# Kernel tuning notes

Measured on AMD Instinct MI355X. Metric: run time of the kernel, lower is better.

Reference implementation:

```python
import jax, jax.numpy as jnp
import numpy as np

B, S, D = 2, 2048, 1024
H, HKV, HD = 16, 4, 64
REP = H // HKV
THETA = 10000.0
NEG = -1e9


def _rope_tables(seq_len, head_dim, theta):
    inv = 1.0 / (theta ** (np.arange(0, head_dim, 2, dtype=np.float32) / head_dim))
    t = np.arange(seq_len, dtype=np.float32)
    f = np.outer(t, inv)  # [S, HD/2]
    return jnp.asarray(np.cos(f)), jnp.asarray(np.sin(f))


def setup_inputs() -> dict:
    key = jax.random.key(0)
    kx, kq, kk, kv, ko = jax.random.split(key, 5)
    s = 0.02
    x = jax.random.normal(kx, (B, S, D), dtype=jnp.float32)
    wq = jax.random.normal(kq, (H * HD, D), dtype=jnp.float32) * s
    wk = jax.random.normal(kk, (HKV * HD, D), dtype=jnp.float32) * s
    wv = jax.random.normal(kv, (HKV * HD, D), dtype=jnp.float32) * s
    wo = jax.random.normal(ko, (D, H * HD), dtype=jnp.float32) * s
    freqs_cos, freqs_sin = _rope_tables(S, HD, THETA)
    mask = jnp.triu(jnp.full((S, S), NEG, dtype=jnp.float32), k=1)  # causal additive
    return {"x": x, "wq": wq, "wk": wk, "wv": wv, "wo": wo,
            "freqs_cos": freqs_cos, "freqs_sin": freqs_sin, "mask": mask}


def _apply_rope(t, cos, sin):
    # t: [B, S, nH, HD]; treat last dim as HD/2 complex pairs, multiply by e^{i f}
    tf = t.astype(jnp.float32).reshape(*t.shape[:-1], HD // 2, 2)
    tr, ti = tf[..., 0], tf[..., 1]
    c = cos[None, :, None, :]
    s = sin[None, :, None, :]
    outr = tr * c - ti * s
    outi = tr * s + ti * c
    out = jnp.stack([outr, outi], axis=-1).reshape(*t.shape)
    return out.astype(t.dtype)


def reference(x, wq, wk, wv, wo, freqs_cos, freqs_sin, mask):
    xq = jnp.einsum('bsd,od->bso', x, wq).reshape(B, S, H, HD)
    xk = jnp.einsum('bsd,od->bso', x, wk).reshape(B, S, HKV, HD)
    xv = jnp.einsum('bsd,od->bso', x, wv).reshape(B, S, HKV, HD)
    xq = _apply_rope(xq, freqs_cos, freqs_sin)
    xk = _apply_rope(xk, freqs_cos, freqs_sin)
    # GQA: group query heads [B,S,HKV,REP,HD]; broadcast KV instead of physical repeat
    xqg = xq.reshape(B, S, HKV, REP, HD)
    scores = jnp.einsum('bqgrd,bkgd->bgrqk', xqg, xk) / jnp.sqrt(jnp.float32(HD))
    scores = scores + mask[None, None, None, :, :]
    attn = jax.nn.softmax(scores.astype(jnp.float32), axis=-1).astype(xq.dtype)
    out = jnp.einsum('bgrqk,bkgd->bqgrd', attn, xv)  # [B,S,HKV,REP,HD]
    out = out.reshape(B, S, H * HD)
    return jnp.einsum('bso,do->bsd', out, wo)
```

## Files before the change

kernel.cpp:

```cpp
#include <hip/hip_runtime.h>


#define B_   2
#define S_   2048
#define D_   1024
#define H_   16
#define HKV_ 4
#define HD_  64

typedef __attribute__((ext_vector_type(8))) short bf16x8;
typedef __attribute__((ext_vector_type(4))) float f32x4;
typedef __attribute__((ext_vector_type(4))) short short4v;

__device__ __forceinline__ short f2bf(float f) {
    unsigned u = __builtin_bit_cast(unsigned, f);
    u += 0x7fffu + ((u >> 16) & 1u);
    return (short)(u >> 16);
}

__device__ __forceinline__ void gll16(const void* g, void* l) {
    __builtin_amdgcn_global_load_lds(
        (const __attribute__((address_space(1))) unsigned int*)g,
        (__attribute__((address_space(3))) unsigned int*)l, 16, 0, 0);
}

__global__ void cast_f32_bf16(const float* __restrict__ in, short* __restrict__ out, int n) {
    int i = (blockIdx.x * blockDim.x + threadIdx.x) * 4;
    if (i >= n) return;
    float4 v = *(const float4*)(in + i);
    short4v o = { f2bf(v.x), f2bf(v.y), f2bf(v.z), f2bf(v.w) };
    *(short4v*)(out + i) = o;
}

__global__ void rope_cast(const float* __restrict__ xqkv, short* __restrict__ out,
                          const float* __restrict__ fc, const float* __restrict__ fs,
                          int nh, int colofs) {
    int idx = blockIdx.x * blockDim.x + threadIdx.x;
    int p    = idx & 31;
    int rest = idx >> 5;
    int h    = rest & (nh - 1);
    int s    = (rest / nh) & (S_ - 1);
    int b    = rest / (nh * S_);
    size_t row = (size_t)b * S_ + s;
    const float* src = xqkv + row * 1536 + colofs + h * 64 + 2 * p;
    float tr = src[0], ti = src[1];
    float c = fc[s * 32 + p], sn = fs[s * 32 + p];
    short* dst = out + (row * nh + h) * 64 + 2 * p;
    dst[0] = f2bf(tr * c - ti * sn);
    dst[1] = f2bf(tr * sn + ti * c);
}

__global__ __launch_bounds__(256) void transpose_cast_v(const float* __restrict__ xqkv,
                                                        short* __restrict__ vt) {
    __shared__ float tl[64][65];
    const int t = threadIdx.x;
    const int s0 = blockIdx.x * 64, g = blockIdx.y, b = blockIdx.z;
#pragma unroll
    for (int i = 0; i < 16; ++i) {
        int e = t + i * 256, r = e >> 6, d = e & 63;
        tl[r][d] = xqkv[(size_t)(b * S_ + s0 + r) * 1536 + 1280 + g * 64 + d];
    }
    __syncthreads();
#pragma unroll
    for (int i = 0; i < 16; ++i) {
        int e = t + i * 256, dr = e >> 6, sc = e & 63;
        vt[(size_t)((b * HKV_ + g) * 64 + dr) * S_ + s0 + sc] = f2bf(tl[sc][dr]);
    }
}

__global__ __launch_bounds__(256, 2) void gemm_bf16_nt(
    const short* __restrict__ A, const short* __restrict__ Bw,
    float* __restrict__ C, int N, int K) {
    __shared__ short A_l[128 * 64];
    __shared__ short B_l[128 * 64];
    const int t = threadIdx.x, ln = t & 63, wid = t >> 6;
    const int wr = wid >> 1, wc = wid & 1;
    const int r0 = blockIdx.y * 128, c0 = blockIdx.x * 128;
    f32x4 acc[4][4] = {};
    for (int k0 = 0; k0 < K; k0 += 64) {
#pragma unroll
        for (int i = 0; i < 4; ++i) {
            int row = wid * 32 + i * 8 + (ln >> 3);
            int sc_ = ((ln & 7) ^ (row & 7)) * 8;
            gll16(A + (size_t)(r0 + row) * K + k0 + sc_, A_l + wid * 2048 + i * 512);
            gll16(Bw + (size_t)(c0 + row) * K + k0 + sc_, B_l + wid * 2048 + i * 512);
        }
        __syncthreads();
#pragma unroll
        for (int kk = 0; kk < 2; ++kk) {
            bf16x8 af[4], bfr[4];
#pragma unroll
            for (int mi = 0; mi < 4; ++mi) {
                int row = wr * 64 + mi * 16 + (ln & 15);
                int addr = row * 128 + (((kk * 4 + (ln >> 4)) ^ (row & 7)) << 4);
                af[mi] = *(const bf16x8*)((const char*)A_l + addr);
            }
#pragma unroll
            for (int ni = 0; ni < 4; ++ni) {
                int col = wc * 64 + ni * 16 + (ln & 15);
                int addr = col * 128 + (((kk * 4 + (ln >> 4)) ^ (col & 7)) << 4);
                bfr[ni] = *(const bf16x8*)((const char*)B_l + addr);
            }
#pragma unroll
            for (int mi = 0; mi < 4; ++mi)
#pragma unroll
                for (int ni = 0; ni < 4; ++ni)
                    acc[mi][ni] = __builtin_amdgcn_mfma_f32_16x16x32_bf16(
                        af[mi], bfr[ni], acc[mi][ni], 0, 0, 0);
        }
        __syncthreads();
    }
#pragma unroll
    for (int mi = 0; mi < 4; ++mi)
#pragma unroll
        for (int ni = 0; ni < 4; ++ni)
#pragma unroll
            for (int rg = 0; rg < 4; ++rg) {
                int r = r0 + wr * 64 + mi * 16 + (ln >> 4) * 4 + rg;
                int c = c0 + wc * 64 + ni * 16 + (ln & 15);
                C[(size_t)r * N + c] = acc[mi][ni][rg];
            }
}

__global__ __launch_bounds__(256, 2) void attn_mfma(
    const short* __restrict__ Qb, const short* __restrict__ Kb,
    const short* __restrict__ Vt, short* __restrict__ Ob) {
    __shared__ short K_l[64 * 64];
    __shared__ short V_l[64 * 64];
    __shared__ short P_l[4 * 16 * 64];
    const int t = threadIdx.x, ln = t & 63, wid = t >> 6;
    const int qt = (int)gridDim.x - 1 - (int)blockIdx.x;
    const int h = blockIdx.y, b = blockIdx.z, g = h >> 2;
    const int q0 = qt * 64;
    const int lg = ln >> 4, q = ln & 15;
    const int qrow = q0 + wid * 16 + q;

    bf16x8 qf[2];
#pragma unroll
    for (int kk = 0; kk < 2; ++kk)
        qf[kk] = *(const bf16x8*)(Qb + ((size_t)(b * S_ + qrow) * H_ + h) * HD_ + kk * 32 + lg * 8);

    f32x4 acc[4] = {};
    float mrun = -3.0e38f, lsum = 0.f;

    for (int kt = 0; kt <= qt; ++kt) {
        const int k0 = kt * 64;
#pragma unroll
        for (int i = 0; i < 2; ++i) {
            int row = wid * 16 + i * 8 + (ln >> 3);
            int sc_ = ((ln & 7) ^ (row & 7)) * 8;
            gll16(Kb + ((size_t)(b * S_ + k0 + row) * HKV_ + g) * HD_ + sc_,
                  K_l + wid * 1024 + i * 512);
            gll16(Vt + ((size_t)((b * HKV_ + g) * 64 + row)) * S_ + k0 + sc_,
                  V_l + wid * 1024 + i * 512);
        }
        __syncthreads();

        f32x4 st[4] = {};
#pragma unroll
        for (int kk = 0; kk < 2; ++kk)
#pragma unroll
            for (int r = 0; r < 4; ++r) {
                int row = r * 16 + q;
                int addr = row * 128 + (((kk * 4 + lg) ^ (row & 7)) << 4);
                bf16x8 ka = *(const bf16x8*)((const char*)K_l + addr);
                st[r] = __builtin_amdgcn_mfma_f32_16x16x32_bf16(ka, qf[kk], st[r], 0, 0, 0);
            }

        const bool diag = (kt == qt);
        const int qg = q0 + wid * 16 + q;
        float mloc = -3.0e38f;
#pragma unroll
        for (int r = 0; r < 4; ++r)
#pragma unroll
            for (int j = 0; j < 4; ++j) {
                float v = st[r][j] * 0.125f;
                if (diag && (k0 + r * 16 + lg * 4 + j > qg)) v = -3.0e38f;
                st[r][j] = v;
                mloc = fmaxf(mloc, v);
            }
        mloc = fmaxf(mloc, __shfl_xor(mloc, 16));
        mloc = fmaxf(mloc, __shfl_xor(mloc, 32));
        float nm = fmaxf(mrun, mloc);
        float scl = __expf(mrun - nm);
        float rsum = 0.f;
#pragma unroll
        for (int r = 0; r < 4; ++r)
#pragma unroll
            for (int j = 0; j < 4; ++j) {
                float e = __expf(st[r][j] - nm);
                st[r][j] = e;
                rsum += e;
            }
        rsum += __shfl_xor(rsum, 16);
        rsum += __shfl_xor(rsum, 32);
        lsum = lsum * scl + rsum;
        mrun = nm;
#pragma unroll
        for (int d = 0; d < 4; ++d)
#pragma unroll
            for (int j = 0; j < 4; ++j) acc[d][j] *= scl;

#pragma unroll
        for (int r = 0; r < 4; ++r) {
            short4v pk = { f2bf(st[r][0]), f2bf(st[r][1]), f2bf(st[r][2]), f2bf(st[r][3]) };
            int sb = wid * 2048 + q * 128 + ((r * 32 + lg * 8) ^ ((q & 7) << 4));
            *(short4v*)((char*)P_l + sb) = pk;
        }

#pragma unroll
        for (int kk2 = 0; kk2 < 2; ++kk2) {
            int pba = wid * 2048 + q * 128 + (((kk2 * 4 + lg) ^ (q & 7)) << 4);
            bf16x8 pb = *(const bf16x8*)((const char*)P_l + pba);
#pragma unroll
            for (int d = 0; d < 4; ++d) {
                int row = d * 16 + q;
                int addr = row * 128 + (((kk2 * 4 + lg) ^ (row & 7)) << 4);
                bf16x8 va = *(const bf16x8*)((const char*)V_l + addr);
                acc[d] = __builtin_amdgcn_mfma_f32_16x16x32_bf16(va, pb, acc[d], 0, 0, 0);
            }
        }
        __syncthreads();
    }

    float inv = 1.f / lsum;
#pragma unroll
    for (int d = 0; d < 4; ++d) {
        short4v o4 = { f2bf(acc[d][0] * inv), f2bf(acc[d][1] * inv),
                       f2bf(acc[d][2] * inv), f2bf(acc[d][3] * inv) };
        *(short4v*)(Ob + ((size_t)(b * S_ + qrow) * H_ + h) * HD_ + d * 16 + lg * 4) = o4;
    }
}

extern "C" void kernel_launch(void* const* d_in, const int* in_sizes, int n_in,
                              void* d_out, int out_size, void* d_ws, size_t ws_size,
                              hipStream_t stream)
{
    const float* x  = (const float*)d_in[0];
    const float* wq = (const float*)d_in[1];
    const float* wk = (const float*)d_in[2];
    const float* wv = (const float*)d_in[3];
    const float* wo = (const float*)d_in[4];
    const float* fc = (const float*)d_in[5];
    const float* fs = (const float*)d_in[6];
    float* out = (float*)d_out;

    char* ws = (char*)d_ws;
    short* wqkvb = (short*)(ws);
    short* wob   = (short*)(ws + 3145728);
    short* xb    = (short*)(ws + 5242880);
    float* xqkv  = (float*)(ws + 13631488);
    short* qb    = (short*)(ws + 38797312);
    short* kb    = (short*)(ws + 47185920);
    short* vtb   = (short*)(ws + 49283072);
    short* aob   = xb;

    cast_f32_bf16<<<4096, 256, 0, stream>>>(x,  xb,               4194304);
    cast_f32_bf16<<<1024, 256, 0, stream>>>(wq, wqkvb,            1048576);
    cast_f32_bf16<<<256,  256, 0, stream>>>(wk, wqkvb + 1048576,  262144);
    cast_f32_bf16<<<256,  256, 0, stream>>>(wv, wqkvb + 1310720,  262144);
    cast_f32_bf16<<<1024, 256, 0, stream>>>(wo, wob,              1048576);

    gemm_bf16_nt<<<dim3(12, 32), 256, 0, stream>>>(xb, wqkvb, xqkv, 1536, 1024);

    rope_cast<<<8192, 256, 0, stream>>>(xqkv, qb, fc, fs, 16, 0);
    rope_cast<<<2048, 256, 0, stream>>>(xqkv, kb, fc, fs, 4, 1024);
    transpose_cast_v<<<dim3(32, 4, 2), 256, 0, stream>>>(xqkv, vtb);

    attn_mfma<<<dim3(32, 16, 2), 256, 0, stream>>>(qb, kb, vtb, aob);

    gemm_bf16_nt<<<dim3(8, 32), 256, 0, stream>>>(aob, wob, out, 1024, 1024);
}
```

Baseline: 224.7 us.

## Fuse casts, fuse RoPE into QKV GEMM epilogue, double-buffer attention KV loads

New measurement: 212.3 us. 5.5% less time.

```diff
diff --git a/kernel.cpp b/kernel.cpp
--- a/kernel.cpp
+++ b/kernel.cpp
@@ -24,47 +24,122 @@
         (__attribute__((address_space(3))) unsigned int*)l, 16, 0, 0);
 }
 
-__global__ void cast_f32_bf16(const float* __restrict__ in, short* __restrict__ out, int n) {
-    int i = (blockIdx.x * blockDim.x + threadIdx.x) * 4;
-    if (i >= n) return;
-    float4 v = *(const float4*)(in + i);
+__global__ void cast_all(const float* __restrict__ x,  const float* __restrict__ wq,
+                         const float* __restrict__ wk, const float* __restrict__ wv,
+                         const float* __restrict__ wo,
+                         short* __restrict__ xb, short* __restrict__ wqkvb,
+                         short* __restrict__ wob) {
+    int i4 = blockIdx.x * blockDim.x + threadIdx.x;
+    const float* src;
+    short* dst;
+    int base;
+    if (i4 < 1048576)      { src = x;  dst = xb;    base = 0; }
+    else if (i4 < 1310720) { src = wq; dst = wqkvb; base = 1048576; }
+    else if (i4 < 1376256) { src = wk; dst = wqkvb + 1048576; base = 1310720; }
+    else if (i4 < 1441792) { src = wv; dst = wqkvb + 1310720; base = 1376256; }
+    else                   { src = wo; dst = wob;   base = 1441792; }
+    int e = (i4 - base) * 4;
+    float4 v = *(const float4*)(src + e);
     short4v o = { f2bf(v.x), f2bf(v.y), f2bf(v.z), f2bf(v.w) };
-    *(short4v*)(out + i) = o;
-}
-
-__global__ void rope_cast(const float* __restrict__ xqkv, short* __restrict__ out,
-                          const float* __restrict__ fc, const float* __restrict__ fs,
-                          int nh, int colofs) {
-    int idx = blockIdx.x * blockDim.x + threadIdx.x;
-    int p    = idx & 31;
-    int rest = idx >> 5;
-    int h    = rest & (nh - 1);
-    int s    = (rest / nh) & (S_ - 1);
-    int b    = rest / (nh * S_);
-    size_t row = (size_t)b * S_ + s;
-    const float* src = xqkv + row * 1536 + colofs + h * 64 + 2 * p;
-    float tr = src[0], ti = src[1];
-    float c = fc[s * 32 + p], sn = fs[s * 32 + p];
-    short* dst = out + (row * nh + h) * 64 + 2 * p;
-    dst[0] = f2bf(tr * c - ti * sn);
-    dst[1] = f2bf(tr * sn + ti * c);
-}
-
-__global__ __launch_bounds__(256) void transpose_cast_v(const float* __restrict__ xqkv,
-                                                        short* __restrict__ vt) {
-    __shared__ float tl[64][65];
+    *(short4v*)(dst + e) = o;
+}
+
+__global__ __launch_bounds__(256, 2) void gemm_qkv(
+    const short* __restrict__ A, const short* __restrict__ W,
+    const float* __restrict__ fc, const float* __restrict__ fs,
+    short* __restrict__ qb, short* __restrict__ kb, short* __restrict__ vb) {
+    __shared__ short A_l[128 * 64];
+    __shared__ short B_l[128 * 64];
+    const int t = threadIdx.x, ln = t & 63, wid = t >> 6;
+    const int wr = wid >> 1, wc = wid & 1;
+    const int r0 = blockIdx.y * 128, c0 = blockIdx.x * 128;
+    const int K = 1024;
+    f32x4 acc[4][4] = {};
+    for (int k0 = 0; k0 < K; k0 += 64) {
+#pragma unroll
+        for (int i = 0; i < 4; ++i) {
+            int row = wid * 32 + i * 8 + (ln >> 3);
+            int sc_ = ((ln & 7) ^ (row & 7)) * 8;
+            gll16(A + (size_t)(r0 + row) * K + k0 + sc_, A_l + wid * 2048 + i * 512);
+            gll16(W + (size_t)(c0 + row) * K + k0 + sc_, B_l + wid * 2048 + i * 512);
+        }
+        __syncthreads();
+#pragma unroll
+        for (int kk = 0; kk < 2; ++kk) {
+            bf16x8 af[4], bfr[4];
+#pragma unroll
+            for (int mi = 0; mi < 4; ++mi) {
+                int row = wr * 64 + mi * 16 + (ln & 15);
+                int addr = row * 128 + (((kk * 4 + (ln >> 4)) ^ (row & 7)) << 4);
+                af[mi] = *(const bf16x8*)((const char*)A_l + addr);
+            }
+#pragma unroll
+            for (int ni = 0; ni < 4; ++ni) {
+                int col = wc * 64 + ni * 16 + (ln & 15);
+                int addr = col * 128 + (((kk * 4 + (ln >> 4)) ^ (col & 7)) << 4);
+                bfr[ni] = *(const bf16x8*)((const char*)B_l + addr);
+            }
+#pragma unroll
+            for (int mi = 0; mi < 4; ++mi)
+#pragma unroll
+                for (int ni = 0; ni < 4; ++ni)
+                    acc[mi][ni] = __builtin_amdgcn_mfma_f32_16x16x32_bf16(
+                        af[mi], bfr[ni], acc[mi][ni], 0, 0, 0);
+        }
+        __syncthreads();
+    }
+
+    const float QSCALE = 0.18033688f;
+    const int region = (c0 < 1024) ? 0 : (c0 < 1280 ? 1 : 2);
+#pragma unroll
+    for (int mi = 0; mi < 4; ++mi)
+#pragma unroll
+        for (int ni = 0; ni < 4; ++ni) {
+            int col = c0 + wc * 64 + ni * 16 + (ln & 15);
+#pragma unroll
+            for (int rg = 0; rg < 4; ++rg) {
+                int row = r0 + wr * 64 + mi * 16 + (ln >> 4) * 4 + rg;
+                int s = row & (S_ - 1), b = row >> 11;
+                float v = acc[mi][ni][rg];
+                if (region == 2) {
+                    int cc = col - 1280, g = cc >> 6, d = cc & 63;
+                    vb[((size_t)(b * S_ + s) * HKV_ + g) * HD_ + d] = f2bf(v);
+                } else {
+                    int cc = region ? (col - 1024) : col;
+                    int d = cc & 63, p = d >> 1;
+                    float c = fc[s * 32 + p], sn = fs[s * 32 + p];
+                    float pv = __shfl_xor(v, 1);
+                    float sgn = (col & 1) ? sn : -sn;
+                    float o = v * c + sgn * pv;
+                    if (region == 0) {
+                        o *= QSCALE;
+                        qb[((size_t)(b * S_ + s) * H_ + (cc >> 6)) * HD_ + d] = f2bf(o);
+                    } else {
+                        kb[((size_t)(b * S_ + s) * HKV_ + (cc >> 6)) * HD_ + d] = f2bf(o);
+                    }
+                }
+            }
+        }
+}
+
+__global__ __launch_bounds__(256) void transpose_v(const short* __restrict__ vb,
+                                                   short* __restrict__ vt) {
+    __shared__ short tl[64][68];
     const int t = threadIdx.x;
     const int s0 = blockIdx.x * 64, g = blockIdx.y, b = blockIdx.z;
 #pragma unroll
-    for (int i = 0; i < 16; ++i) {
-        int e = t + i * 256, r = e >> 6, d = e & 63;
-        tl[r][d] = xqkv[(size_t)(b * S_ + s0 + r) * 1536 + 1280 + g * 64 + d];
+    for (int i = 0; i < 4; ++i) {
+        int e = t + i * 256, r = e >> 4, c4 = (e & 15) * 4;
+        *(short4v*)&tl[r][c4] =
+            *(const short4v*)(vb + ((size_t)(b * S_ + s0 + r) * HKV_ + g) * HD_ + c4);
     }
     __syncthreads();
-#pragma unroll
-    for (int i = 0; i < 16; ++i) {
-        int e = t + i * 256, dr = e >> 6, sc = e & 63;
-        vt[(size_t)((b * HKV_ + g) * 64 + dr) * S_ + s0 + sc] = f2bf(tl[sc][dr]);
+    const int dr = t >> 2, sc0 = (t & 3) * 16;
+#pragma unroll
+    for (int i = 0; i < 4; ++i) {
+        short4v o = { tl[sc0 + i * 4 + 0][dr], tl[sc0 + i * 4 + 1][dr],
+                      tl[sc0 + i * 4 + 2][dr], tl[sc0 + i * 4 + 3][dr] };
+        *(short4v*)(vt + ((size_t)((b * HKV_ + g) * 64 + dr)) * S_ + s0 + sc0 + i * 4) = o;
     }
 }
 
@@ -122,18 +197,20 @@
             }
 }
 
-__global__ __launch_bounds__(256, 2) void attn_mfma(
+__global__ __launch_bounds__(256, 4) void attn_mfma(
     const short* __restrict__ Qb, const short* __restrict__ Kb,
     const short* __restrict__ Vt, short* __restrict__ Ob) {
-    __shared__ short K_l[64 * 64];
-    __shared__ short V_l[64 * 64];
-    __shared__ short P_l[4 * 16 * 64];
+    __shared__ short K_l[2][64 * 64];
+    __shared__ short V_l[2][64 * 64];
+    __shared__ short P_l[4][16 * 64];
     const int t = threadIdx.x, ln = t & 63, wid = t >> 6;
     const int qt = (int)gridDim.x - 1 - (int)blockIdx.x;
     const int h = blockIdx.y, b = blockIdx.z, g = h >> 2;
     const int q0 = qt * 64;
     const int lg = ln >> 4, q = ln & 15;
     const int qrow = q0 + wid * 16 + q;
+    const int stg_row = wid * 16 + (ln >> 3);
+    const int stg_sc0 = (ln & 7) * 8;
 
     bf16x8 qf[2];
 #pragma unroll
@@ -143,19 +220,28 @@
     f32x4 acc[4] = {};
     float mrun = -3.0e38f, lsum = 0.f;
 
+#define STAGE(KT, BUF)                                                              \
+    {                                                                               \
+        const int k0s = (KT) * 64;                                                  \
+        _Pragma("unroll")                                                           \
+        for (int i = 0; i < 2; ++i) {                                               \
+            int row = stg_row + i * 8;                                              \
+            int sc_ = stg_sc0 ^ ((row & 7) * 8);                                    \
+            gll16(Kb + ((size_t)(b * S_ + k0s + row) * HKV_ + g) * HD_ + sc_,       \
+                  &K_l[BUF][wid * 1024 + i * 512]);                                 \
+            gll16(Vt + ((size_t)((b * HKV_ + g) * 64 + row)) * S_ + k0s + sc_,      \
+                  &V_l[BUF][wid * 1024 + i * 512]);                                 \
+        }                                                                           \
+    }
+
+    STAGE(0, 0);
+    __syncthreads();
+    int cur = 0;
+
     for (int kt = 0; kt <= qt; ++kt) {
+        if (kt < qt) STAGE(kt + 1, cur ^ 1);
+
         const int k0 = kt * 64;
-#pragma unroll
-        for (int i = 0; i < 2; ++i) {
-            int row = wid * 16 + i * 8 + (ln >> 3);
-            int sc_ = ((ln & 7) ^ (row & 7)) * 8;
-            gll16(Kb + ((size_t)(b * S_ + k0 + row) * HKV_ + g) * HD_ + sc_,
-                  K_l + wid * 1024 + i * 512);
-            gll16(Vt + ((size_t)((b * HKV_ + g) * 64 + row)) * S_ + k0 + sc_,
-                  V_l + wid * 1024 + i * 512);
-        }
-        __syncthreads();
-
         f32x4 st[4] = {};
 #pragma unroll
         for (int kk = 0; kk < 2; ++kk)
@@ -163,65 +249,76 @@
             for (int r = 0; r < 4; ++r) {
                 int row = r * 16 + q;
                 int addr = row * 128 + (((kk * 4 + lg) ^ (row & 7)) << 4);
-                bf16x8 ka = *(const bf16x8*)((const char*)K_l + addr);
+                bf16x8 ka = *(const bf16x8*)((const char*)&K_l[cur][0] + addr);
                 st[r] = __builtin_amdgcn_mfma_f32_16x16x32_bf16(ka, qf[kk], st[r], 0, 0, 0);
             }
 
         const bool diag = (kt == qt);
-        const int qg = q0 + wid * 16 + q;
         float mloc = -3.0e38f;
-#pragma unroll
-        for (int r = 0; r < 4; ++r)
-#pragma unroll
-            for (int j = 0; j < 4; ++j) {
-                float v = st[r][j] * 0.125f;
-                if (diag && (k0 + r * 16 + lg * 4 + j > qg)) v = -3.0e38f;
-                st[r][j] = v;
-                mloc = fmaxf(mloc, v);
-            }
+        if (diag) {
+#pragma unroll
+            for (int r = 0; r < 4; ++r)
+#pragma unroll
+                for (int j = 0; j < 4; ++j) {
+                    if (k0 + r * 16 + lg * 4 + j > qrow) st[r][j] = -3.0e38f;
+                    mloc = fmaxf(mloc, st[r][j]);
+                }
+        } else {
+#pragma unroll
+            for (int r = 0; r < 4; ++r)
+#pragma unroll
+                for (int j = 0; j < 4; ++j) mloc = fmaxf(mloc, st[r][j]);
+        }
         mloc = fmaxf(mloc, __shfl_xor(mloc, 16));
         mloc = fmaxf(mloc, __shfl_xor(mloc, 32));
-        float nm = fmaxf(mrun, mloc);
-        float scl = __expf(mrun - nm);
+
+        if (!__all(mloc <= mrun + 8.f)) {
+            float nm = fmaxf(mrun, mloc);
+            float scl = __builtin_amdgcn_exp2f(mrun - nm);
+            lsum *= scl;
+#pragma unroll
+            for (int d = 0; d < 4; ++d)
+#pragma unroll
+                for (int j = 0; j < 4; ++j) acc[d][j] *= scl;
+            mrun = nm;
+        }
+
         float rsum = 0.f;
 #pragma unroll
         for (int r = 0; r < 4; ++r)
 #pragma unroll
             for (int j = 0; j < 4; ++j) {
-                float e = __expf(st[r][j] - nm);
+                float e = __builtin_amdgcn_exp2f(st[r][j] - mrun);
                 st[r][j] = e;
                 rsum += e;
             }
         rsum += __shfl_xor(rsum, 16);
         rsum += __shfl_xor(rsum, 32);
-        lsum = lsum * scl + rsum;
-        mrun = nm;
-#pragma unroll
-        for (int d = 0; d < 4; ++d)
-#pragma unroll
-            for (int j = 0; j < 4; ++j) acc[d][j] *= scl;
+        lsum += rsum;
 
 #pragma unroll
         for (int r = 0; r < 4; ++r) {
             short4v pk = { f2bf(st[r][0]), f2bf(st[r][1]), f2bf(st[r][2]), f2bf(st[r][3]) };
-            int sb = wid * 2048 + q * 128 + ((r * 32 + lg * 8) ^ ((q & 7) << 4));
-            *(short4v*)((char*)P_l + sb) = pk;
+            int sb = q * 128 + ((r * 32 + lg * 8) ^ ((q & 7) << 4));
+            *(short4v*)((char*)&P_l[wid][0] + sb) = pk;
         }
 
 #pragma unroll
         for (int kk2 = 0; kk2 < 2; ++kk2) {
-            int pba = wid * 2048 + q * 128 + (((kk2 * 4 + lg) ^ (q & 7)) << 4);
-            bf16x8 pb = *(const bf16x8*)((const char*)P_l + pba);
+            int pba = q * 128 + (((kk2 * 4 + lg) ^ (q & 7)) << 4);
+            bf16x8 pb = *(const bf16x8*)((const char*)&P_l[wid][0] + pba);
 #pragma unroll
             for (int d = 0; d < 4; ++d) {
                 int row = d * 16 + q;
                 int addr = row * 128 + (((kk2 * 4 + lg) ^ (row & 7)) << 4);
-                bf16x8 va = *(const bf16x8*)((const char*)V_l + addr);
+                bf16x8 va = *(const bf16x8*)((const char*)&V_l[cur][0] + addr);
                 acc[d] = __builtin_amdgcn_mfma_f32_16x16x32_bf16(va, pb, acc[d], 0, 0, 0);
             }
         }
         __syncthreads();
-    }
+        cur ^= 1;
+    }
+#undef STAGE
 
     float inv = 1.f / lsum;
 #pragma unroll
@@ -249,23 +346,17 @@
     short* wqkvb = (short*)(ws);
     short* wob   = (short*)(ws + 3145728);
     short* xb    = (short*)(ws + 5242880);
-    float* xqkv  = (float*)(ws + 13631488);
-    short* qb    = (short*)(ws + 38797312);
-    short* kb    = (short*)(ws + 47185920);
-    short* vtb   = (short*)(ws + 49283072);
+    short* qb    = (short*)(ws + 13631488);
+    short* kb    = (short*)(ws + 22020096);
+    short* vb    = (short*)(ws + 24117248);
+    short* vtb   = (short*)(ws + 26214400);
     short* aob   = xb;
 
-    cast_f32_bf16<<<4096, 256, 0, stream>>>(x,  xb,               4194304);
-    cast_f32_bf16<<<1024, 256, 0, stream>>>(wq, wqkvb,            1048576);
-    cast_f32_bf16<<<256,  256, 0, stream>>>(wk, wqkvb + 1048576,  262144);
-    cast_f32_bf16<<<256,  256, 0, stream>>>(wv, wqkvb + 1310720,  262144);
-    cast_f32_bf16<<<1024, 256, 0, stream>>>(wo, wob,              1048576);
-
-    gemm_bf16_nt<<<dim3(12, 32), 256, 0, stream>>>(xb, wqkvb, xqkv, 1536, 1024);
-
-    rope_cast<<<8192, 256, 0, stream>>>(xqkv, qb, fc, fs, 16, 0);
-    rope_cast<<<2048, 256, 0, stream>>>(xqkv, kb, fc, fs, 4, 1024);
-    transpose_cast_v<<<dim3(32, 4, 2), 256, 0, stream>>>(xqkv, vtb);
+    cast_all<<<6656, 256, 0, stream>>>(x, wq, wk, wv, wo, xb, wqkvb, wob);
+
+    gemm_qkv<<<dim3(12, 32), 256, 0, stream>>>(xb, wqkvb, fc, fs, qb, kb, vb);
+
+    transpose_v<<<dim3(32, 4, 2), 256, 0, stream>>>(vb, vtb);
 
     attn_mfma<<<dim3(32, 16, 2), 256, 0, stream>>>(qb, kb, vtb, aob);
 
```
